# Performance work log

Hardware: AMD Instinct MI355X
Metric: run time of the kernel (lower is better)

Reference implementation:

```python
import jax, jax.numpy as jnp
import numpy as np

B, L, N, D = 16, 4096, 512, 256
EPS = 1e-8  # torch F.cosine_similarity default eps


def setup_inputs() -> dict:
    key = jax.random.key(0)
    k1, k2, k3 = jax.random.split(key, 3)
    spk_decoder_out = jax.random.normal(k1, (B, L, D), dtype=jnp.float32)
    profile = jax.random.normal(k2, (B, N, D), dtype=jnp.float32)
    # lengths in [1, N] so every batch has at least one valid profile
    profile_lens = jax.random.randint(k3, (B,), 1, N + 1, dtype=jnp.int32)
    return {"spk_decoder_out": spk_decoder_out, "profile": profile,
            "profile_lens": profile_lens}


def reference(spk_decoder_out, profile, profile_lens):
    # cosine similarity between (B,L,1,D) and (B,1,N,D) along D, computed
    # without materializing the (B,L,N,D) broadcast intermediate
    dots = jnp.einsum('bld,bnd->bln', spk_decoder_out, profile)      # (B,L,N)
    x_norm = jnp.sqrt(jnp.sum(spk_decoder_out * spk_decoder_out, axis=-1))  # (B,L)
    p_norm = jnp.sqrt(jnp.sum(profile * profile, axis=-1))           # (B,N)
    denom = jnp.maximum(x_norm[:, :, None] * p_norm[:, None, :], EPS)
    sim = dots / denom                                               # (B,L,N)

    # pad mask over profiles: True where n >= profile_lens[b]
    n = profile.shape[1]
    mask = jnp.arange(n, dtype=profile_lens.dtype)[None, :] >= profile_lens[:, None]  # (B,N)
    min_value = jnp.finfo(jnp.float32).min
    sim = jnp.where(mask[:, None, :], min_value, sim)
    weights = jax.nn.softmax(sim, axis=-1)
    weights = jnp.where(mask[:, None, :], 0.0, weights)              # (B,L,N)

    spk_embedding = jnp.einsum('bln,bnd->bld', weights, profile)     # (B,L,D)
    return spk_embedding, weights
```

## Files before the change

### kernel.cpp

```cpp
#include <hip/hip_runtime.h>
#include <hip/hip_bf16.h>
#include <math.h>

#define BB 16
#define LL 4096
#define NN 512
#define DD 256

typedef __attribute__((ext_vector_type(8))) short  bf16x8;
typedef __attribute__((ext_vector_type(4))) float  f32x4;
typedef __attribute__((ext_vector_type(4))) unsigned short u16x4;

typedef __attribute__((address_space(1))) const void  gvoid_t;
typedef __attribute__((address_space(3))) void        lvoid_t;

__device__ __forceinline__ unsigned short f2bf(float x) {
    union { float f; unsigned u; } v; v.f = x;
    unsigned r = v.u + 0x7fffu + ((v.u >> 16) & 1u);
    return (unsigned short)(r >> 16);
}
__device__ __forceinline__ float bfhi(unsigned u) { return __uint_as_float(u & 0xffff0000u); }
__device__ __forceinline__ float bflo(unsigned u) { return __uint_as_float(u << 16); }

__global__ __launch_bounds__(256) void cda_prep(
    const float* __restrict__ P, char* __restrict__ pnI, char* __restrict__ peI)
{
    const int gw   = blockIdx.x * 4 + (threadIdx.x >> 6);
    const int lane = threadIdx.x & 63;
    const float4 v = *(const float4*)(P + (size_t)gw * DD + lane * 4);
    float ss = v.x * v.x + v.y * v.y + v.z * v.z + v.w * v.w;
    #pragma unroll
    for (int off = 32; off > 0; off >>= 1) ss += __shfl_xor(ss, off);
    const float rinv = 1.0f / sqrtf(ss);
    const int n  = gw & (NN - 1);
    const int nl = n & 31;
    const size_t tile = ((size_t)((gw >> 9) * 16 + (n >> 5))) << 14;

    u16x4 h;
    h.x = f2bf(v.x * rinv); h.y = f2bf(v.y * rinv);
    h.z = f2bf(v.z * rinv); h.w = f2bf(v.w * rinv);
    *(u16x4*)(pnI + tile + ((nl * 512 + lane * 8) ^ ((nl & 7) << 4))) = h;

    const int ks = ((nl >> 2) & 3) * 8 + ((nl >> 4) << 2) + (nl & 3);
    const float raw[4] = {v.x, v.y, v.z, v.w};
    #pragma unroll
    for (int j = 0; j < 4; ++j) {
        const int d = lane * 4 + j;
        *(unsigned short*)(peI + tile + ((d * 64 + ks * 2) ^ ((d & 15) << 4))) = f2bf(raw[j]);
    }
}

struct __align__(16) Smem {
    union {
        struct { char pn[2][16384]; char pe[2][16384]; } img;
        char xstage[32768];
    } u;
    float wtile[64 * 36];
    float tbl[64];
};

__global__ __launch_bounds__(256, 2) void cda_main(
    const float* __restrict__ X, const char* __restrict__ pnI,
    const char* __restrict__ peI, const int* __restrict__ lens,
    float* __restrict__ out)
{
    __shared__ Smem sm;

    const int id = blockIdx.x;
    const int b  = (id & 7) * 2 + (id >> 9);
    const int l0 = ((id >> 3) & 63) * 64;

    const int tid  = threadIdx.x;
    const int w    = tid >> 6;
    const int lane = tid & 63;
    const int lo   = lane & 15;
    const int g    = lane >> 4;
    const int len  = lens[b];

    const float* Xb  = X + ((size_t)b * LL + l0) * DD;
    const char*  pnB = pnI + (size_t)b * 262144;
    const char*  peB = peI + (size_t)b * 262144;

    #pragma unroll
    for (int rr = 0; rr < 16; ++rr) {
        const int row = w * 16 + rr;
        const float4 v = *(const float4*)(Xb + row * DD + lane * 4);
        float ss = v.x * v.x + v.y * v.y + v.z * v.z + v.w * v.w;
        #pragma unroll
        for (int off = 32; off > 0; off >>= 1) ss += __shfl_xor(ss, off);
        const float inv = 1.0f / sqrtf(ss);
        u16x4 h;
        h.x = f2bf(v.x * inv); h.y = f2bf(v.y * inv);
        h.z = f2bf(v.z * inv); h.w = f2bf(v.w * inv);
        *(u16x4*)(sm.u.xstage + ((row * 512 + lane * 8) ^ ((row & 7) << 4))) = h;
    }
    __syncthreads();
    bf16x8 xf[8];
    #pragma unroll
    for (int ks = 0; ks < 8; ++ks)
        xf[ks] = *(const bf16x8*)(sm.u.xstage +
            (((w * 16 + lo) * 512 + ks * 64 + g * 16) ^ ((lo & 7) << 4)));
    __syncthreads();

    #pragma unroll
    for (int q = 0; q < 4; ++q)
        __builtin_amdgcn_global_load_lds((gvoid_t*)(pnB + q * 4096 + tid * 16),
                                         (lvoid_t*)(sm.u.img.pn[0] + q * 4096 + tid * 16), 16, 0, 0);
    #pragma unroll
    for (int q = 0; q < 4; ++q)
        __builtin_amdgcn_global_load_lds((gvoid_t*)(peB + q * 4096 + tid * 16),
                                         (lvoid_t*)(sm.u.img.pe[0] + q * 4096 + tid * 16), 16, 0, 0);

    f32x4 e[16];
    #pragma unroll
    for (int i = 0; i < 16; ++i) e[i] = (f32x4){0.f, 0.f, 0.f, 0.f};
    unsigned pm[16][4];
    float ssum = 0.f;

    #pragma unroll
    for (int c = 0; c < 16; ++c) {
        const int pb = c & 1;
        asm volatile("s_waitcnt vmcnt(0)" ::: "memory");
        __builtin_amdgcn_s_barrier();
        __builtin_amdgcn_sched_barrier(0);
        if (c < 15) {
            const char* pnT = pnB + (c + 1) * 16384;
            const char* peT = peB + (c + 1) * 16384;
            char* pnD = sm.u.img.pn[pb ^ 1];
            char* peD = sm.u.img.pe[pb ^ 1];
            #pragma unroll
            for (int q = 0; q < 4; ++q)
                __builtin_amdgcn_global_load_lds((gvoid_t*)(pnT + q * 4096 + tid * 16),
                                                 (lvoid_t*)(pnD + q * 4096 + tid * 16), 16, 0, 0);
            #pragma unroll
            for (int q = 0; q < 4; ++q)
                __builtin_amdgcn_global_load_lds((gvoid_t*)(peT + q * 4096 + tid * 16),
                                                 (lvoid_t*)(peD + q * 4096 + tid * 16), 16, 0, 0);
        }

        const char* pnL = sm.u.img.pn[pb];
        f32x4 a0 = (f32x4){0.f, 0.f, 0.f, 0.f};
        f32x4 a1 = (f32x4){0.f, 0.f, 0.f, 0.f};
        #pragma unroll
        for (int ks = 0; ks < 8; ++ks) {
            const bf16x8 f0 = *(const bf16x8*)(pnL +
                ((lo * 512 + ks * 64 + g * 16) ^ ((lo & 7) << 4)));
            a0 = __builtin_amdgcn_mfma_f32_16x16x32_bf16(f0, xf[ks], a0, 0, 0, 0);
            const bf16x8 f1 = *(const bf16x8*)(pnL +
                (((16 + lo) * 512 + ks * 64 + g * 16) ^ ((lo & 7) << 4)));
            a1 = __builtin_amdgcn_mfma_f32_16x16x32_bf16(f1, xf[ks], a1, 0, 0, 0);
        }

        unsigned short pw[8];
        #pragma unroll
        for (int r = 0; r < 4; ++r) {
            const int n0 = c * 32 + g * 4 + r;
            const float p0 = (n0 < len) ? __expf(a0[r]) : 0.f;
            ssum += p0; pw[r] = f2bf(p0);
            const float p1 = (n0 + 16 < len) ? __expf(a1[r]) : 0.f;
            ssum += p1; pw[4 + r] = f2bf(p1);
        }
        pm[c][0] = (unsigned)pw[0] | ((unsigned)pw[1] << 16);
        pm[c][1] = (unsigned)pw[2] | ((unsigned)pw[3] << 16);
        pm[c][2] = (unsigned)pw[4] | ((unsigned)pw[5] << 16);
        pm[c][3] = (unsigned)pw[6] | ((unsigned)pw[7] << 16);

        union { unsigned u[4]; bf16x8 v; } pf;
        pf.u[0] = pm[c][0]; pf.u[1] = pm[c][1]; pf.u[2] = pm[c][2]; pf.u[3] = pm[c][3];
        const char* peL = sm.u.img.pe[pb];
        #pragma unroll
        for (int df = 0; df < 16; ++df) {
            const bf16x8 bf = *(const bf16x8*)(peL +
                (((df * 16 + lo) * 64 + g * 16) ^ (lo << 4)));
            e[df] = __builtin_amdgcn_mfma_f32_16x16x32_bf16(pf.v, bf, e[df], 0, 0, 0);
        }
    }

    ssum += __shfl_xor(ssum, 16);
    ssum += __shfl_xor(ssum, 32);
    const float sinv = 1.0f / ssum;
    if (g == 0) sm.tbl[w * 16 + lo] = sinv;

    float* Wout = out + (size_t)BB * LL * DD + ((size_t)b * LL + l0) * (size_t)NN;
    #pragma unroll
    for (int c = 0; c < 16; ++c) {
        float4 v0, v1;
        v0.x = bflo(pm[c][0]) * sinv; v0.y = bfhi(pm[c][0]) * sinv;
        v0.z = bflo(pm[c][1]) * sinv; v0.w = bfhi(pm[c][1]) * sinv;
        v1.x = bflo(pm[c][2]) * sinv; v1.y = bfhi(pm[c][2]) * sinv;
        v1.z = bflo(pm[c][3]) * sinv; v1.w = bfhi(pm[c][3]) * sinv;
        char* base = (char*)sm.wtile + (size_t)(w * 16 + lo) * 144 + g * 16;
        *(float4*)(base)      = v0;
        *(float4*)(base + 64) = v1;
        asm volatile("s_waitcnt lgkmcnt(0)" ::: "memory");
        __builtin_amdgcn_s_barrier();
        #pragma unroll
        for (int i = 0; i < 2; ++i) {
            const int slot = tid + 256 * i;
            const int row = slot >> 3, grp = slot & 7;
            const float4 t = *(const float4*)((char*)sm.wtile + (size_t)row * 144 + grp * 16);
            *(float4*)(Wout + (size_t)(l0 ? 0 : 0) + (size_t)row * NN + c * 32 + grp * 4) = t;
        }
        asm volatile("s_waitcnt lgkmcnt(0)" ::: "memory");
        __builtin_amdgcn_s_barrier();
    }

    float t4[4];
    #pragma unroll
    for (int r = 0; r < 4; ++r) t4[r] = sm.tbl[w * 16 + g * 4 + r];
    char* scr = sm.u.img.pe[0] + w * 4096;
    float* Eout = out + ((size_t)b * LL + l0 + w * 16) * DD;
    #pragma unroll
    for (int r = 0; r < 4; ++r) {
        #pragma unroll
        for (int df = 0; df < 16; ++df)
            *(float*)(scr + g * 1024 + (size_t)(df * 16 + lo) * 4) = e[df][r] * t4[r];
        #pragma unroll
        for (int it = 0; it < 4; ++it) {
            const float4 t = *(const float4*)(scr + it * 1024 + lane * 16);
            *(float4*)(Eout + (size_t)(it * 4 + r) * DD + lane * 4) = t;
        }
    }
}

extern "C" void kernel_launch(void* const* d_in, const int* in_sizes, int n_in,
                              void* d_out, int out_size, void* d_ws, size_t ws_size,
                              hipStream_t stream) {
    const float* X    = (const float*)d_in[0];
    const float* P    = (const float*)d_in[1];
    const int*   lens = (const int*)d_in[2];
    float*       out  = (float*)d_out;

    char* pnI = (char*)d_ws;
    char* peI = (char*)d_ws + 4194304;

    hipLaunchKernelGGL(cda_prep, dim3(BB * NN / 4), dim3(256), 0, stream, P, pnI, peI);
    hipLaunchKernelGGL(cda_main, dim3(1024), dim3(256), 0, stream, X, pnI, peI, lens, out);
}
```

Measured before the change: 102.1 us.

## Split fused loop into score phase and PV phase with separate prefetch

Splits the single loop, which streamed both the normalized and raw profile tiles, into two phases. The first computes all scores and exponentials while double-buffering only the normalized tiles. The second double-buffers the raw tiles while writing the weights straight to global memory and accumulating the embedding MFMAs. This shrinks shared memory per block, drops the weight staging tile and its per-chunk barriers, moves the first profile prefetch ahead of the X normalization, and pads the epilogue scratch stride to avoid bank conflicts. In exchange, each global weight store is now a 16-byte write per lane rather than a coalesced tile store, and the e accumulators stay live only in the second phase, which changes register pressure.

```diff
diff --git a/kernel.cpp b/kernel.cpp
--- a/kernel.cpp
+++ b/kernel.cpp
@@ -13,6 +13,8 @@
 
 typedef __attribute__((address_space(1))) const void  gvoid_t;
 typedef __attribute__((address_space(3))) void        lvoid_t;
+
+#define GLL16(src, dst) __builtin_amdgcn_global_load_lds((gvoid_t*)(src), (lvoid_t*)(dst), 16, 0, 0)
 
 __device__ __forceinline__ unsigned short f2bf(float x) {
     union { float f; unsigned u; } v; v.f = x;
@@ -51,11 +53,11 @@
 }
 
 struct __align__(16) Smem {
+    char pn[2][16384];
     union {
-        struct { char pn[2][16384]; char pe[2][16384]; } img;
         char xstage[32768];
+        char pe[2][16384];
     } u;
-    float wtile[64 * 36];
     float tbl[64];
 };
 
@@ -82,6 +84,10 @@
     const char*  peB = peI + (size_t)b * 262144;
 
     #pragma unroll
+    for (int q = 0; q < 4; ++q)
+        GLL16(pnB + q * 4096 + tid * 16, (char*)sm.pn[0] + q * 4096 + tid * 16);
+
+    #pragma unroll
     for (int rr = 0; rr < 16; ++rr) {
         const int row = w * 16 + rr;
         const float4 v = *(const float4*)(Xb + row * DD + lane * 4);
@@ -104,41 +110,24 @@
 
     #pragma unroll
     for (int q = 0; q < 4; ++q)
-        __builtin_amdgcn_global_load_lds((gvoid_t*)(pnB + q * 4096 + tid * 16),
-                                         (lvoid_t*)(sm.u.img.pn[0] + q * 4096 + tid * 16), 16, 0, 0);
-    #pragma unroll
-    for (int q = 0; q < 4; ++q)
-        __builtin_amdgcn_global_load_lds((gvoid_t*)(peB + q * 4096 + tid * 16),
-                                         (lvoid_t*)(sm.u.img.pe[0] + q * 4096 + tid * 16), 16, 0, 0);
-
-    f32x4 e[16];
-    #pragma unroll
-    for (int i = 0; i < 16; ++i) e[i] = (f32x4){0.f, 0.f, 0.f, 0.f};
+        GLL16(peB + q * 4096 + tid * 16, (char*)sm.u.pe[0] + q * 4096 + tid * 16);
+
     unsigned pm[16][4];
     float ssum = 0.f;
 
     #pragma unroll
     for (int c = 0; c < 16; ++c) {
-        const int pb = c & 1;
         asm volatile("s_waitcnt vmcnt(0)" ::: "memory");
         __builtin_amdgcn_s_barrier();
         __builtin_amdgcn_sched_barrier(0);
         if (c < 15) {
-            const char* pnT = pnB + (c + 1) * 16384;
-            const char* peT = peB + (c + 1) * 16384;
-            char* pnD = sm.u.img.pn[pb ^ 1];
-            char* peD = sm.u.img.pe[pb ^ 1];
+            const char* src = pnB + (c + 1) * 16384;
+            char* dst = (char*)sm.pn[(c + 1) & 1];
             #pragma unroll
             for (int q = 0; q < 4; ++q)
-                __builtin_amdgcn_global_load_lds((gvoid_t*)(pnT + q * 4096 + tid * 16),
-                                                 (lvoid_t*)(pnD + q * 4096 + tid * 16), 16, 0, 0);
-            #pragma unroll
-            for (int q = 0; q < 4; ++q)
-                __builtin_amdgcn_global_load_lds((gvoid_t*)(peT + q * 4096 + tid * 16),
-                                                 (lvoid_t*)(peD + q * 4096 + tid * 16), 16, 0, 0);
-        }
-
-        const char* pnL = sm.u.img.pn[pb];
+                GLL16(src + q * 4096 + tid * 16, dst + q * 4096 + tid * 16);
+        }
+        const char* pnL = (const char*)sm.pn[c & 1];
         f32x4 a0 = (f32x4){0.f, 0.f, 0.f, 0.f};
         f32x4 a1 = (f32x4){0.f, 0.f, 0.f, 0.f};
         #pragma unroll
@@ -150,7 +139,6 @@
                 (((16 + lo) * 512 + ks * 64 + g * 16) ^ ((lo & 7) << 4)));
             a1 = __builtin_amdgcn_mfma_f32_16x16x32_bf16(f1, xf[ks], a1, 0, 0, 0);
         }
-
         unsigned short pw[8];
         #pragma unroll
         for (int r = 0; r < 4; ++r) {
@@ -164,16 +152,6 @@
         pm[c][1] = (unsigned)pw[2] | ((unsigned)pw[3] << 16);
         pm[c][2] = (unsigned)pw[4] | ((unsigned)pw[5] << 16);
         pm[c][3] = (unsigned)pw[6] | ((unsigned)pw[7] << 16);
-
-        union { unsigned u[4]; bf16x8 v; } pf;
-        pf.u[0] = pm[c][0]; pf.u[1] = pm[c][1]; pf.u[2] = pm[c][2]; pf.u[3] = pm[c][3];
-        const char* peL = sm.u.img.pe[pb];
-        #pragma unroll
-        for (int df = 0; df < 16; ++df) {
-            const bf16x8 bf = *(const bf16x8*)(peL +
-                (((df * 16 + lo) * 64 + g * 16) ^ (lo << 4)));
-            e[df] = __builtin_amdgcn_mfma_f32_16x16x32_bf16(pf.v, bf, e[df], 0, 0, 0);
-        }
     }
 
     ssum += __shfl_xor(ssum, 16);
@@ -181,43 +159,59 @@
     const float sinv = 1.0f / ssum;
     if (g == 0) sm.tbl[w * 16 + lo] = sinv;
 
-    float* Wout = out + (size_t)BB * LL * DD + ((size_t)b * LL + l0) * (size_t)NN;
+    f32x4 e[16];
+    #pragma unroll
+    for (int i = 0; i < 16; ++i) e[i] = (f32x4){0.f, 0.f, 0.f, 0.f};
+
+    float* Wrow = out + (size_t)BB * LL * DD
+                + ((size_t)b * LL + l0 + w * 16 + lo) * (size_t)NN;
+
     #pragma unroll
     for (int c = 0; c < 16; ++c) {
+        if (c == 0) asm volatile("s_waitcnt vmcnt(0)" ::: "memory");
+        else        asm volatile("s_waitcnt vmcnt(2)" ::: "memory");
+        __builtin_amdgcn_s_barrier();
+        __builtin_amdgcn_sched_barrier(0);
+        if (c < 15) {
+            const char* src = peB + (c + 1) * 16384;
+            char* dst = (char*)sm.u.pe[(c + 1) & 1];
+            #pragma unroll
+            for (int q = 0; q < 4; ++q)
+                GLL16(src + q * 4096 + tid * 16, dst + q * 4096 + tid * 16);
+        }
         float4 v0, v1;
         v0.x = bflo(pm[c][0]) * sinv; v0.y = bfhi(pm[c][0]) * sinv;
         v0.z = bflo(pm[c][1]) * sinv; v0.w = bfhi(pm[c][1]) * sinv;
         v1.x = bflo(pm[c][2]) * sinv; v1.y = bfhi(pm[c][2]) * sinv;
         v1.z = bflo(pm[c][3]) * sinv; v1.w = bfhi(pm[c][3]) * sinv;
-        char* base = (char*)sm.wtile + (size_t)(w * 16 + lo) * 144 + g * 16;
-        *(float4*)(base)      = v0;
-        *(float4*)(base + 64) = v1;
-        asm volatile("s_waitcnt lgkmcnt(0)" ::: "memory");
-        __builtin_amdgcn_s_barrier();
-        #pragma unroll
-        for (int i = 0; i < 2; ++i) {
-            const int slot = tid + 256 * i;
-            const int row = slot >> 3, grp = slot & 7;
-            const float4 t = *(const float4*)((char*)sm.wtile + (size_t)row * 144 + grp * 16);
-            *(float4*)(Wout + (size_t)(l0 ? 0 : 0) + (size_t)row * NN + c * 32 + grp * 4) = t;
-        }
-        asm volatile("s_waitcnt lgkmcnt(0)" ::: "memory");
-        __builtin_amdgcn_s_barrier();
+        *(float4*)(Wrow + c * 32 + g * 4)      = v0;
+        *(float4*)(Wrow + c * 32 + 16 + g * 4) = v1;
+
+        union { unsigned u[4]; bf16x8 v; } pf;
+        pf.u[0] = pm[c][0]; pf.u[1] = pm[c][1];
+        pf.u[2] = pm[c][2]; pf.u[3] = pm[c][3];
+        const char* peL = (const char*)sm.u.pe[c & 1];
+        #pragma unroll
+        for (int df = 0; df < 16; ++df) {
+            const bf16x8 bf = *(const bf16x8*)(peL +
+                (((df * 16 + lo) * 64 + g * 16) ^ (lo << 4)));
+            e[df] = __builtin_amdgcn_mfma_f32_16x16x32_bf16(pf.v, bf, e[df], 0, 0, 0);
+        }
     }
 
     float t4[4];
     #pragma unroll
     for (int r = 0; r < 4; ++r) t4[r] = sm.tbl[w * 16 + g * 4 + r];
-    char* scr = sm.u.img.pe[0] + w * 4096;
+    char* scr = (char*)sm.pn + w * 8192;
     float* Eout = out + ((size_t)b * LL + l0 + w * 16) * DD;
     #pragma unroll
     for (int r = 0; r < 4; ++r) {
         #pragma unroll
         for (int df = 0; df < 16; ++df)
-            *(float*)(scr + g * 1024 + (size_t)(df * 16 + lo) * 4) = e[df][r] * t4[r];
+            *(float*)(scr + g * 1040 + (size_t)(df * 16 + lo) * 4) = e[df][r] * t4[r];
         #pragma unroll
         for (int it = 0; it < 4; ++it) {
-            const float4 t = *(const float4*)(scr + it * 1024 + lane * 16);
+            const float4 t = *(const float4*)(scr + it * 1040 + lane * 16);
             *(float4*)(Eout + (size_t)(it * 4 + r) * DD + lane * 4) = t;
         }
     }
```

Result: faster. 96.40 us (-5.6%).
